# Kernel tuning notes

Hardware: AMD Instinct MI355X
Metric: run time of the kernel (lower is better)

The kernel has to match this reference:

```python
import jax, jax.numpy as jnp
import numpy as np

B, T, I, H = 128, 128, 12, 512


def setup_inputs() -> dict:
    key = jax.random.key(0)
    k1, k2, k3, k4 = jax.random.split(key, 4)
    s_ih = 1.0 / np.sqrt(H)
    return {
        "history": jax.random.normal(k1, (B, T, I), dtype=jnp.float32),
        "W_ih": jax.random.uniform(k2, (3 * H, I), dtype=jnp.float32, minval=-s_ih, maxval=s_ih),
        "W_hh": jax.random.uniform(k3, (3 * H, H), dtype=jnp.float32, minval=-s_ih, maxval=s_ih),
        "W_pred": jax.random.uniform(k4, (2, H), dtype=jnp.float32, minval=-s_ih, maxval=s_ih),
    }


def reference(history, W_ih, W_hh, W_pred):
    # GRUCell (bias=False), PyTorch gate order: r, z, n
    def step(h, x_t):
        gi = x_t @ W_ih.T            # [B, 3H]
        gh = h @ W_hh.T              # [B, 3H]
        i_r, i_z, i_n = jnp.split(gi, 3, axis=-1)
        h_r, h_z, h_n = jnp.split(gh, 3, axis=-1)
        r = jax.nn.sigmoid(i_r + h_r)
        z = jax.nn.sigmoid(i_z + h_z)
        n = jnp.tanh(i_n + r * h_n)
        h_new = (1.0 - z) * n + z * h
        logit = h_new @ W_pred.T     # per-step bubble_prediction head
        return h_new, logit

    h0 = jnp.zeros((history.shape[0], W_hh.shape[1]), dtype=history.dtype)
    xs = jnp.swapaxes(history, 0, 1)          # [T, B, I]
    h_last, logits_tbf = jax.lax.scan(step, h0, xs)
    logits = jnp.swapaxes(logits_tbf, 0, 1)   # [B, T, 2]
    return logits, h_last
```

## Files before the change

### kernel.cpp

```cpp
#include <hip/hip_runtime.h>
#include <cstdint>


typedef __attribute__((ext_vector_type(4))) float f32x4;
typedef __attribute__((ext_vector_type(8))) __bf16 bf16x8;

#define NTHREADS 256
#define CG_N 32
#define BB 16
#define HC 16
#define T_STEPS 128
#define I_DIM 12
#define H_DIM 512

#define WS_HX0   0
#define WS_HX1   262144
#define WS_FLAGS 524288

__device__ __forceinline__ float bf16f(unsigned short u){
  return __uint_as_float(((unsigned int)u) << 16);
}

__device__ __forceinline__ void split_bf16(float x, unsigned short &hi, unsigned short &lo){
  unsigned int u = __float_as_uint(x);
  hi = (unsigned short)(u >> 16);
  float r = x - __uint_as_float((u >> 16) << 16);
  unsigned int ru = __float_as_uint(r);
  ru += 0x7fffu + ((ru >> 16) & 1u);
  lo = (unsigned short)(ru >> 16);
}

__device__ __forceinline__ float fsigmoid(float x){ return 1.0f / (1.0f + __expf(-x)); }
__device__ __forceinline__ float ftanh(float x){ return 2.0f / (1.0f + __expf(-2.0f * x)) - 1.0f; }

__device__ __forceinline__ f32x4 MFMA(bf16x8 a, bf16x8 b, f32x4 c){
  return __builtin_amdgcn_mfma_f32_16x16x32_bf16(a, b, c, 0, 0, 0);
}

__device__ __forceinline__ void dev_store_u32(unsigned int* p, unsigned int v){
  asm volatile("global_store_dword %0, %1, off sc1" :: "v"(p), "v"(v) : "memory");
}
__device__ __forceinline__ unsigned int dev_load_u32(const unsigned int* p){
  unsigned int v;
  asm volatile("global_load_dword %0, %1, off sc1\n\t"
               "s_waitcnt vmcnt(0)" : "=v"(v) : "v"(p) : "memory");
  return v;
}
__device__ __forceinline__ void wait_vm0(){
  asm volatile("s_waitcnt vmcnt(0)" ::: "memory");
}

__device__ __forceinline__ unsigned int hiP(unsigned int x, unsigned int y){
  return (x >> 16) | (y & 0xFFFF0000u);
}
__device__ __forceinline__ unsigned int loP(unsigned int x, unsigned int y){
  return (x & 0xFFFFu) | (y << 16);
}

extern "C" __global__ void __launch_bounds__(NTHREADS, 1)
gru_persistent(const float* __restrict__ hist, const float* __restrict__ wih,
               const float* __restrict__ whh, const float* __restrict__ wpred,
               float* __restrict__ out, unsigned char* __restrict__ ws)
{
  __shared__ __align__(16) unsigned short whi_l[3*16*64*8];
  __shared__ __align__(16) unsigned short wlo_l[3*16*64*8];
  __shared__ __align__(16) unsigned short hhi_l[BB*H_DIM];
  __shared__ __align__(16) unsigned short hlo_l[BB*H_DIM];
  __shared__ __align__(16) float part_l[4*3*64*4];
  __shared__ __align__(16) float x_l[BB*I_DIM];
  __shared__ __align__(16) float wih_l[48*I_DIM];
  __shared__ __align__(16) float wpred_l[2*H_DIM];

  const int tid  = threadIdx.x;
  const int bg   = blockIdx.x & 7;
  const int cg   = blockIdx.x >> 3;
  const int wave = tid >> 6;
  const int lane = tid & 63;

  unsigned int* hx[2] = {(unsigned int*)(ws + WS_HX0), (unsigned int*)(ws + WS_HX1)};
  unsigned int* flagsP = (unsigned int*)(ws + WS_FLAGS);

  for (int i = tid; i < 48*I_DIM; i += NTHREADS){
    int j = i / I_DIM, ii = i % I_DIM;
    int R = (j >> 4)*H_DIM + cg*HC + (j & 15);
    wih_l[i] = wih[R*I_DIM + ii];
  }
  if (cg < 4){
    for (int i = tid; i < 2*H_DIM; i += NTHREADS) wpred_l[i] = wpred[i];
  }
  #pragma unroll
  for (int it = 0; it < 24; ++it){
    int f0 = (it*NTHREADS + tid) * 4;
    int j = f0 >> 9, k = f0 & 511;
    int R = (j >> 4)*H_DIM + cg*HC + (j & 15);
    float4 v = *(const float4*)(whh + R*H_DIM + k);
    int nt = j >> 4;
    int ln = (j & 15) | (((k >> 3) & 3) << 4);
    int kt = k >> 5, e = k & 7;
    int base = (((nt*16 + kt)*64) + ln)*8 + e;
    float vv[4] = {v.x, v.y, v.z, v.w};
    unsigned short h4[4], l4[4];
    #pragma unroll
    for (int q = 0; q < 4; ++q) split_bf16(vv[q], h4[q], l4[q]);
    uint2 uh, ul;
    uh.x = (unsigned int)h4[0] | ((unsigned int)h4[1] << 16);
    uh.y = (unsigned int)h4[2] | ((unsigned int)h4[3] << 16);
    ul.x = (unsigned int)l4[0] | ((unsigned int)l4[1] << 16);
    ul.y = (unsigned int)l4[2] | ((unsigned int)l4[3] << 16);
    *(uint2*)((char*)whi_l + base*2) = uh;
    *(uint2*)((char*)wlo_l + base*2) = ul;
  }

  {
    int b = tid >> 4, hc = tid & 15;
    dev_store_u32(hx[0] + (bg*BB + b)*H_DIM + cg*HC + hc, 0u);
  }
  wait_vm0();
  __syncthreads();
  if (wave == 0 && lane < CG_N)
    dev_store_u32(flagsP + (bg*CG_N + lane)*CG_N + cg, 1u);
  if (wave == 0){
    const unsigned int* fp = flagsP + (bg*CG_N + cg)*CG_N + (lane & 31);
    for (;;){
      unsigned int f = dev_load_u32(fp);
      if (__ballot(f >= 1u) == ~0ull) break;
      __builtin_amdgcn_s_sleep(1);
    }
  }
  __syncthreads();

  for (int t = 0; t < T_STEPS; ++t){
    const int cur = t & 1, nxt = cur ^ 1;

    if (tid < BB*I_DIM){
      int b = tid / I_DIM, ii = tid % I_DIM;
      x_l[tid] = hist[((bg*BB + b)*T_STEPS + t)*I_DIM + ii];
    }

    {
      int row = tid & 15, col0 = (tid >> 4) * 32;
      const unsigned int* p = hx[cur] + (bg*BB + row)*H_DIM + col0;
      uint4 v0, v1, v2, v3, v4, v5, v6, v7;
      asm volatile(
        "global_load_dwordx4 %0, %8, off sc1\n\t"
        "global_load_dwordx4 %1, %8, off offset:16 sc1\n\t"
        "global_load_dwordx4 %2, %8, off offset:32 sc1\n\t"
        "global_load_dwordx4 %3, %8, off offset:48 sc1\n\t"
        "global_load_dwordx4 %4, %8, off offset:64 sc1\n\t"
        "global_load_dwordx4 %5, %8, off offset:80 sc1\n\t"
        "global_load_dwordx4 %6, %8, off offset:96 sc1\n\t"
        "global_load_dwordx4 %7, %8, off offset:112 sc1\n\t"
        "s_waitcnt vmcnt(0)"
        : "=&v"(v0), "=&v"(v1), "=&v"(v2), "=&v"(v3),
          "=&v"(v4), "=&v"(v5), "=&v"(v6), "=&v"(v7)
        : "v"(p) : "memory");
      uint4 pr[8] = {v0, v1, v2, v3, v4, v5, v6, v7};
      #pragma unroll
      for (int k = 0; k < 4; ++k){
        uint4 a = pr[2*k], b = pr[2*k+1];
        uint4 hi4 = { hiP(a.x,a.y), hiP(a.z,a.w), hiP(b.x,b.y), hiP(b.z,b.w) };
        uint4 lo4 = { loP(a.x,a.y), loP(a.z,a.w), loP(b.x,b.y), loP(b.z,b.w) };
        int boff = row*1024 + (((col0 + 8*k)*2) ^ ((row & 7) << 4));
        *(uint4*)((char*)hhi_l + boff) = hi4;
        *(uint4*)((char*)hlo_l + boff) = lo4;
      }
    }
    __syncthreads();

    if (cg < 4 && t > 0){
      int o = cg & 1;
      int b = ((cg >> 1) << 3) + (tid >> 5);
      int s = tid & 31;
      float p = 0.f;
      #pragma unroll
      for (int q = 0; q < 2; ++q){
        int c = s*16 + q*8;
        int boff = b*1024 + ((c*2) ^ ((b & 7) << 4));
        uint4 vh = *(const uint4*)((const char*)hhi_l + boff);
        uint4 vl = *(const uint4*)((const char*)hlo_l + boff);
        const unsigned short* ph = (const unsigned short*)&vh;
        const unsigned short* pl = (const unsigned short*)&vl;
        #pragma unroll
        for (int e = 0; e < 8; ++e)
          p += (bf16f(ph[e]) + bf16f(pl[e])) * wpred_l[o*H_DIM + c + e];
      }
      #pragma unroll
      for (int m = 1; m < 32; m <<= 1) p += __shfl_xor(p, m);
      if (s == 0) out[((bg*BB + b)*T_STEPS + (t-1))*2 + o] = p;
    }

    f32x4 acc[3];
    #pragma unroll
    for (int nt = 0; nt < 3; ++nt) acc[nt] = {0.f, 0.f, 0.f, 0.f};
    #pragma unroll
    for (int kk = 0; kk < 4; ++kk){
      int kt = wave*4 + kk;
      int arow = lane & 15;
      int aboff = arow*1024 + ((kt*64 + (lane >> 4)*16) ^ ((arow & 7) << 4));
      bf16x8 ahi = *(const bf16x8*)((const char*)hhi_l + aboff);
      bf16x8 alo = *(const bf16x8*)((const char*)hlo_l + aboff);
      #pragma unroll
      for (int nt = 0; nt < 3; ++nt){
        int bboff = (((nt*16 + kt)*64) + lane)*16;
        bf16x8 bhi = *(const bf16x8*)((const char*)whi_l + bboff);
        bf16x8 blo = *(const bf16x8*)((const char*)wlo_l + bboff);
        acc[nt] = MFMA(ahi, bhi, acc[nt]);
        acc[nt] = MFMA(ahi, blo, acc[nt]);
        acc[nt] = MFMA(alo, bhi, acc[nt]);
      }
    }
    #pragma unroll
    for (int nt = 0; nt < 3; ++nt)
      *(f32x4*)(part_l + ((wave*3 + nt)*64 + lane)*4) = acc[nt];
    __syncthreads();

    {
      int b = tid >> 4, hc = tid & 15;
      int lc = ((b >> 2) << 4) | hc;
      int rc = b & 3;
      float gh[3];
      #pragma unroll
      for (int g = 0; g < 3; ++g){
        float s = 0.f;
        #pragma unroll
        for (int w = 0; w < 4; ++w) s += part_l[((w*3 + g)*64 + lc)*4 + rc];
        gh[g] = s;
      }
      float gi[3];
      #pragma unroll
      for (int g = 0; g < 3; ++g){
        float s = 0.f;
        #pragma unroll
        for (int ii = 0; ii < I_DIM; ++ii)
          s += x_l[b*I_DIM + ii] * wih_l[(g*16 + hc)*I_DIM + ii];
        gi[g] = s;
      }
      float r = fsigmoid(gi[0] + gh[0]);
      float z = fsigmoid(gi[1] + gh[1]);
      float n = ftanh(gi[2] + r*gh[2]);
      int colg = cg*HC + hc;
      int hoff = b*1024 + ((colg*2) ^ ((b & 7) << 4));
      float hp = bf16f(*(unsigned short*)((char*)hhi_l + hoff))
               + bf16f(*(unsigned short*)((char*)hlo_l + hoff));
      float hn = (1.0f - z)*n + z*hp;

      unsigned short shi, slo; split_bf16(hn, shi, slo);
      unsigned int pk = ((unsigned int)shi << 16) | (unsigned int)slo;
      int gidx = (bg*BB + b)*H_DIM + colg;
      dev_store_u32(hx[nxt] + gidx, pk);
      if (t == T_STEPS - 1) out[32768 + gidx] = hn;
    }

    wait_vm0();
    __syncthreads();
    {
      const unsigned int target = (unsigned int)(t + 2);
      if (wave == 0 && lane < CG_N)
        dev_store_u32(flagsP + (bg*CG_N + lane)*CG_N + cg, target);
      if (wave == 0){
        const unsigned int* fp = flagsP + (bg*CG_N + cg)*CG_N + (lane & 31);
        for (;;){
          unsigned int f = dev_load_u32(fp);
          if (__ballot(f >= target) == ~0ull) break;
          __builtin_amdgcn_s_sleep(1);
        }
      }
    }
    __syncthreads();
  }

  if (cg < 4){
    int row = tid & 15, col0 = (tid >> 4) * 32;
    const unsigned int* p = hx[0] + (bg*BB + row)*H_DIM + col0;
    uint4 v0, v1, v2, v3, v4, v5, v6, v7;
    asm volatile(
      "global_load_dwordx4 %0, %8, off sc1\n\t"
      "global_load_dwordx4 %1, %8, off offset:16 sc1\n\t"
      "global_load_dwordx4 %2, %8, off offset:32 sc1\n\t"
      "global_load_dwordx4 %3, %8, off offset:48 sc1\n\t"
      "global_load_dwordx4 %4, %8, off offset:64 sc1\n\t"
      "global_load_dwordx4 %5, %8, off offset:80 sc1\n\t"
      "global_load_dwordx4 %6, %8, off offset:96 sc1\n\t"
      "global_load_dwordx4 %7, %8, off offset:112 sc1\n\t"
      "s_waitcnt vmcnt(0)"
      : "=&v"(v0), "=&v"(v1), "=&v"(v2), "=&v"(v3),
        "=&v"(v4), "=&v"(v5), "=&v"(v6), "=&v"(v7)
      : "v"(p) : "memory");
    uint4 pr[8] = {v0, v1, v2, v3, v4, v5, v6, v7};
    #pragma unroll
    for (int k = 0; k < 4; ++k){
      uint4 a = pr[2*k], b = pr[2*k+1];
      uint4 hi4 = { hiP(a.x,a.y), hiP(a.z,a.w), hiP(b.x,b.y), hiP(b.z,b.w) };
      uint4 lo4 = { loP(a.x,a.y), loP(a.z,a.w), loP(b.x,b.y), loP(b.z,b.w) };
      int boff = row*1024 + (((col0 + 8*k)*2) ^ ((row & 7) << 4));
      *(uint4*)((char*)hhi_l + boff) = hi4;
      *(uint4*)((char*)hlo_l + boff) = lo4;
    }
    __syncthreads();
    int o = cg & 1;
    int b = ((cg >> 1) << 3) + (tid >> 5);
    int s = tid & 31;
    float pacc = 0.f;
    #pragma unroll
    for (int q = 0; q < 2; ++q){
      int c = s*16 + q*8;
      int boff = b*1024 + ((c*2) ^ ((b & 7) << 4));
      uint4 vh = *(const uint4*)((const char*)hhi_l + boff);
      uint4 vl = *(const uint4*)((const char*)hlo_l + boff);
      const unsigned short* ph = (const unsigned short*)&vh;
      const unsigned short* pl = (const unsigned short*)&vl;
      #pragma unroll
      for (int e = 0; e < 8; ++e)
        pacc += (bf16f(ph[e]) + bf16f(pl[e])) * wpred_l[o*H_DIM + c + e];
    }
    #pragma unroll
    for (int m = 1; m < 32; m <<= 1) pacc += __shfl_xor(pacc, m);
    if (s == 0) out[((bg*BB + b)*T_STEPS + 127)*2 + o] = pacc;
  }
}

extern "C" void kernel_launch(void* const* d_in, const int* in_sizes, int n_in,
                              void* d_out, int out_size, void* d_ws, size_t ws_size,
                              hipStream_t stream) {
  const float* hist  = (const float*)d_in[0];
  const float* wih   = (const float*)d_in[1];
  const float* whh   = (const float*)d_in[2];
  const float* wpred = (const float*)d_in[3];
  float* out = (float*)d_out;
  unsigned char* ws = (unsigned char*)d_ws;

  hipMemsetAsync(ws + WS_FLAGS, 0, 8*CG_N*CG_N*4, stream);

  gru_persistent<<<dim3(256), dim3(NTHREADS), 0, stream>>>(hist, wih, whh, wpred, out, ws);
}
```

Measured before the change: 640.5 us.

## Replace flag barrier with step tags embedded in hidden-state words

Drops the per-step flag-array barrier between the 32 column-group blocks. Each block now writes a 2-bit step tag into the low bits of the bf16 low half of every hidden-state word, and readers poll their hidden row until all tags match the expected step. The prediction-head work is also moved after the state store so it runs off the critical path. This removes a full global barrier round trip per step. In exchange it costs 2 bits of precision in the low bf16 and adds spin-polling on the wider state loads.

```diff
diff --git a/kernel.cpp b/kernel.cpp
--- a/kernel.cpp
+++ b/kernel.cpp
@@ -20,7 +20,6 @@
 __device__ __forceinline__ float bf16f(unsigned short u){
   return __uint_as_float(((unsigned int)u) << 16);
 }
-
 __device__ __forceinline__ void split_bf16(float x, unsigned short &hi, unsigned short &lo){
   unsigned int u = __float_as_uint(x);
   hi = (unsigned short)(u >> 16);
@@ -29,32 +28,63 @@
   ru += 0x7fffu + ((ru >> 16) & 1u);
   lo = (unsigned short)(ru >> 16);
 }
-
 __device__ __forceinline__ float fsigmoid(float x){ return 1.0f / (1.0f + __expf(-x)); }
 __device__ __forceinline__ float ftanh(float x){ return 2.0f / (1.0f + __expf(-2.0f * x)) - 1.0f; }
-
 __device__ __forceinline__ f32x4 MFMA(bf16x8 a, bf16x8 b, f32x4 c){
   return __builtin_amdgcn_mfma_f32_16x16x32_bf16(a, b, c, 0, 0, 0);
 }
+__device__ __forceinline__ void wait_vm0(){
+  asm volatile("s_waitcnt vmcnt(0)" ::: "memory");
+}
+__device__ __forceinline__ unsigned int hiP(unsigned int x, unsigned int y){
+  return (x >> 16) | (y & 0xFFFF0000u);
+}
+__device__ __forceinline__ unsigned int loP(unsigned int x, unsigned int y){
+  return (x & 0xFFFFu) | (y << 16);
+}
 
 __device__ __forceinline__ void dev_store_u32(unsigned int* p, unsigned int v){
   asm volatile("global_store_dword %0, %1, off sc1" :: "v"(p), "v"(v) : "memory");
 }
 __device__ __forceinline__ unsigned int dev_load_u32(const unsigned int* p){
   unsigned int v;
-  asm volatile("global_load_dword %0, %1, off sc1\n\t"
-               "s_waitcnt vmcnt(0)" : "=v"(v) : "v"(p) : "memory");
+  asm volatile("global_load_dword %0, %1, off sc1\n\ts_waitcnt vmcnt(0)"
+               : "=v"(v) : "v"(p) : "memory");
   return v;
 }
-__device__ __forceinline__ void wait_vm0(){
-  asm volatile("s_waitcnt vmcnt(0)" ::: "memory");
-}
-
-__device__ __forceinline__ unsigned int hiP(unsigned int x, unsigned int y){
-  return (x >> 16) | (y & 0xFFFF0000u);
-}
-__device__ __forceinline__ unsigned int loP(unsigned int x, unsigned int y){
-  return (x & 0xFFFFu) | (y << 16);
+__device__ __forceinline__ void load_h_row(const unsigned int* p, uint4* pr){
+  uint4 v0, v1, v2, v3, v4, v5, v6, v7;
+  asm volatile(
+    "global_load_dwordx4 %0, %8, off sc1\n\t"
+    "global_load_dwordx4 %1, %8, off offset:16 sc1\n\t"
+    "global_load_dwordx4 %2, %8, off offset:32 sc1\n\t"
+    "global_load_dwordx4 %3, %8, off offset:48 sc1\n\t"
+    "global_load_dwordx4 %4, %8, off offset:64 sc1\n\t"
+    "global_load_dwordx4 %5, %8, off offset:80 sc1\n\t"
+    "global_load_dwordx4 %6, %8, off offset:96 sc1\n\t"
+    "global_load_dwordx4 %7, %8, off offset:112 sc1\n\t"
+    "s_waitcnt vmcnt(0)"
+    : "=&v"(v0), "=&v"(v1), "=&v"(v2), "=&v"(v3),
+      "=&v"(v4), "=&v"(v5), "=&v"(v6), "=&v"(v7)
+    : "v"(p) : "memory");
+  pr[0]=v0; pr[1]=v1; pr[2]=v2; pr[3]=v3; pr[4]=v4; pr[5]=v5; pr[6]=v6; pr[7]=v7;
+}
+
+__device__ __forceinline__ void poll_h_row(const unsigned int* p, uint4* pr,
+                                           unsigned int want){
+  for (;;){
+    load_h_row(p, pr);
+    unsigned int diff = 0u;
+    #pragma unroll
+    for (int b = 0; b < 8; ++b)
+      diff |= (pr[b].x ^ want) | (pr[b].y ^ want) | (pr[b].z ^ want) | (pr[b].w ^ want);
+    if ((diff & 3u) == 0u) break;
+  }
+  #pragma unroll
+  for (int b = 0; b < 8; ++b){
+    pr[b].x &= 0xFFFFFFFCu; pr[b].y &= 0xFFFFFFFCu;
+    pr[b].z &= 0xFFFFFFFCu; pr[b].w &= 0xFFFFFFFCu;
+  }
 }
 
 extern "C" __global__ void __launch_bounds__(NTHREADS, 1)
@@ -113,7 +143,9 @@
 
   {
     int b = tid >> 4, hc = tid & 15;
-    dev_store_u32(hx[0] + (bg*BB + b)*H_DIM + cg*HC + hc, 0u);
+    int gidx = (bg*BB + b)*H_DIM + cg*HC + hc;
+    dev_store_u32(hx[0] + gidx, 0u);
+    dev_store_u32(hx[1] + gidx, 2u);
   }
   wait_vm0();
   __syncthreads();
@@ -140,21 +172,8 @@
     {
       int row = tid & 15, col0 = (tid >> 4) * 32;
       const unsigned int* p = hx[cur] + (bg*BB + row)*H_DIM + col0;
-      uint4 v0, v1, v2, v3, v4, v5, v6, v7;
-      asm volatile(
-        "global_load_dwordx4 %0, %8, off sc1\n\t"
-        "global_load_dwordx4 %1, %8, off offset:16 sc1\n\t"
-        "global_load_dwordx4 %2, %8, off offset:32 sc1\n\t"
-        "global_load_dwordx4 %3, %8, off offset:48 sc1\n\t"
-        "global_load_dwordx4 %4, %8, off offset:64 sc1\n\t"
-        "global_load_dwordx4 %5, %8, off offset:80 sc1\n\t"
-        "global_load_dwordx4 %6, %8, off offset:96 sc1\n\t"
-        "global_load_dwordx4 %7, %8, off offset:112 sc1\n\t"
-        "s_waitcnt vmcnt(0)"
-        : "=&v"(v0), "=&v"(v1), "=&v"(v2), "=&v"(v3),
-          "=&v"(v4), "=&v"(v5), "=&v"(v6), "=&v"(v7)
-        : "v"(p) : "memory");
-      uint4 pr[8] = {v0, v1, v2, v3, v4, v5, v6, v7};
+      uint4 pr[8];
+      poll_h_row(p, pr, (unsigned int)(t & 3));
       #pragma unroll
       for (int k = 0; k < 4; ++k){
         uint4 a = pr[2*k], b = pr[2*k+1];
@@ -166,6 +185,69 @@
       }
     }
     __syncthreads();
+
+    f32x4 acc[3];
+    #pragma unroll
+    for (int nt = 0; nt < 3; ++nt) acc[nt] = {0.f, 0.f, 0.f, 0.f};
+    #pragma unroll
+    for (int kk = 0; kk < 4; ++kk){
+      int kt = wave*4 + kk;
+      int arow = lane & 15;
+      int aboff = arow*1024 + ((kt*64 + (lane >> 4)*16) ^ ((arow & 7) << 4));
+      bf16x8 ahi = *(const bf16x8*)((const char*)hhi_l + aboff);
+      bf16x8 alo = *(const bf16x8*)((const char*)hlo_l + aboff);
+      #pragma unroll
+      for (int nt = 0; nt < 3; ++nt){
+        int bboff = (((nt*16 + kt)*64) + lane)*16;
+        bf16x8 bhi = *(const bf16x8*)((const char*)whi_l + bboff);
+        bf16x8 blo = *(const bf16x8*)((const char*)wlo_l + bboff);
+        acc[nt] = MFMA(ahi, bhi, acc[nt]);
+        acc[nt] = MFMA(ahi, blo, acc[nt]);
+        acc[nt] = MFMA(alo, bhi, acc[nt]);
+      }
+    }
+    #pragma unroll
+    for (int nt = 0; nt < 3; ++nt)
+      *(f32x4*)(part_l + ((wave*3 + nt)*64 + lane)*4) = acc[nt];
+    __syncthreads();
+
+    {
+      int b = tid >> 4, hc = tid & 15;
+      int lc = ((b >> 2) << 4) | hc;
+      int rc = b & 3;
+      float gh[3];
+      #pragma unroll
+      for (int g = 0; g < 3; ++g){
+        float s = 0.f;
+        #pragma unroll
+        for (int w = 0; w < 4; ++w) s += part_l[((w*3 + g)*64 + lc)*4 + rc];
+        gh[g] = s;
+      }
+      float gi[3];
+      #pragma unroll
+      for (int g = 0; g < 3; ++g){
+        float s = 0.f;
+        #pragma unroll
+        for (int ii = 0; ii < I_DIM; ++ii)
+          s += x_l[b*I_DIM + ii] * wih_l[(g*16 + hc)*I_DIM + ii];
+        gi[g] = s;
+      }
+      float r = fsigmoid(gi[0] + gh[0]);
+      float z = fsigmoid(gi[1] + gh[1]);
+      float n = ftanh(gi[2] + r*gh[2]);
+      int colg = cg*HC + hc;
+      int hoff = b*1024 + ((colg*2) ^ ((b & 7) << 4));
+      float hp = bf16f(*(unsigned short*)((char*)hhi_l + hoff))
+               + bf16f(*(unsigned short*)((char*)hlo_l + hoff));
+      float hn = (1.0f - z)*n + z*hp;
+
+      unsigned short shi, slo; split_bf16(hn, shi, slo);
+      unsigned int pk = ((unsigned int)shi << 16) | ((unsigned int)slo & 0xFFFCu)
+                      | (unsigned int)((t + 1) & 3);
+      int gidx = (bg*BB + b)*H_DIM + colg;
+      dev_store_u32(hx[nxt] + gidx, pk);
+      if (t == T_STEPS - 1) out[32768 + gidx] = hn;
+    }
 
     if (cg < 4 && t > 0){
       int o = cg & 1;
@@ -189,104 +271,14 @@
       if (s == 0) out[((bg*BB + b)*T_STEPS + (t-1))*2 + o] = p;
     }
 
-    f32x4 acc[3];
-    #pragma unroll
-    for (int nt = 0; nt < 3; ++nt) acc[nt] = {0.f, 0.f, 0.f, 0.f};
-    #pragma unroll
-    for (int kk = 0; kk < 4; ++kk){
-      int kt = wave*4 + kk;
-      int arow = lane & 15;
-      int aboff = arow*1024 + ((kt*64 + (lane >> 4)*16) ^ ((arow & 7) << 4));
-      bf16x8 ahi = *(const bf16x8*)((const char*)hhi_l + aboff);
-      bf16x8 alo = *(const bf16x8*)((const char*)hlo_l + aboff);
-      #pragma unroll
-      for (int nt = 0; nt < 3; ++nt){
-        int bboff = (((nt*16 + kt)*64) + lane)*16;
-        bf16x8 bhi = *(const bf16x8*)((const char*)whi_l + bboff);
-        bf16x8 blo = *(const bf16x8*)((const char*)wlo_l + bboff);
-        acc[nt] = MFMA(ahi, bhi, acc[nt]);
-        acc[nt] = MFMA(ahi, blo, acc[nt]);
-        acc[nt] = MFMA(alo, bhi, acc[nt]);
-      }
-    }
-    #pragma unroll
-    for (int nt = 0; nt < 3; ++nt)
-      *(f32x4*)(part_l + ((wave*3 + nt)*64 + lane)*4) = acc[nt];
-    __syncthreads();
-
-    {
-      int b = tid >> 4, hc = tid & 15;
-      int lc = ((b >> 2) << 4) | hc;
-      int rc = b & 3;
-      float gh[3];
-      #pragma unroll
-      for (int g = 0; g < 3; ++g){
-        float s = 0.f;
-        #pragma unroll
-        for (int w = 0; w < 4; ++w) s += part_l[((w*3 + g)*64 + lc)*4 + rc];
-        gh[g] = s;
-      }
-      float gi[3];
-      #pragma unroll
-      for (int g = 0; g < 3; ++g){
-        float s = 0.f;
-        #pragma unroll
-        for (int ii = 0; ii < I_DIM; ++ii)
-          s += x_l[b*I_DIM + ii] * wih_l[(g*16 + hc)*I_DIM + ii];
-        gi[g] = s;
-      }
-      float r = fsigmoid(gi[0] + gh[0]);
-      float z = fsigmoid(gi[1] + gh[1]);
-      float n = ftanh(gi[2] + r*gh[2]);
-      int colg = cg*HC + hc;
-      int hoff = b*1024 + ((colg*2) ^ ((b & 7) << 4));
-      float hp = bf16f(*(unsigned short*)((char*)hhi_l + hoff))
-               + bf16f(*(unsigned short*)((char*)hlo_l + hoff));
-      float hn = (1.0f - z)*n + z*hp;
-
-      unsigned short shi, slo; split_bf16(hn, shi, slo);
-      unsigned int pk = ((unsigned int)shi << 16) | (unsigned int)slo;
-      int gidx = (bg*BB + b)*H_DIM + colg;
-      dev_store_u32(hx[nxt] + gidx, pk);
-      if (t == T_STEPS - 1) out[32768 + gidx] = hn;
-    }
-
-    wait_vm0();
-    __syncthreads();
-    {
-      const unsigned int target = (unsigned int)(t + 2);
-      if (wave == 0 && lane < CG_N)
-        dev_store_u32(flagsP + (bg*CG_N + lane)*CG_N + cg, target);
-      if (wave == 0){
-        const unsigned int* fp = flagsP + (bg*CG_N + cg)*CG_N + (lane & 31);
-        for (;;){
-          unsigned int f = dev_load_u32(fp);
-          if (__ballot(f >= target) == ~0ull) break;
-          __builtin_amdgcn_s_sleep(1);
-        }
-      }
-    }
     __syncthreads();
   }
 
   if (cg < 4){
     int row = tid & 15, col0 = (tid >> 4) * 32;
     const unsigned int* p = hx[0] + (bg*BB + row)*H_DIM + col0;
-    uint4 v0, v1, v2, v3, v4, v5, v6, v7;
-    asm volatile(
-      "global_load_dwordx4 %0, %8, off sc1\n\t"
-      "global_load_dwordx4 %1, %8, off offset:16 sc1\n\t"
-      "global_load_dwordx4 %2, %8, off offset:32 sc1\n\t"
-      "global_load_dwordx4 %3, %8, off offset:48 sc1\n\t"
-      "global_load_dwordx4 %4, %8, off offset:64 sc1\n\t"
-      "global_load_dwordx4 %5, %8, off offset:80 sc1\n\t"
-      "global_load_dwordx4 %6, %8, off offset:96 sc1\n\t"
-      "global_load_dwordx4 %7, %8, off offset:112 sc1\n\t"
-      "s_waitcnt vmcnt(0)"
-      : "=&v"(v0), "=&v"(v1), "=&v"(v2), "=&v"(v3),
-        "=&v"(v4), "=&v"(v5), "=&v"(v6), "=&v"(v7)
-      : "v"(p) : "memory");
-    uint4 pr[8] = {v0, v1, v2, v3, v4, v5, v6, v7};
+    uint4 pr[8];
+    poll_h_row(p, pr, 0u);
     #pragma unroll
     for (int k = 0; k < 4; ++k){
       uint4 a = pr[2*k], b = pr[2*k+1];
```

New measurement: 601.4 us. 1.07x faster.
